# Kernel optimization log

Hardware: AMD Instinct MI355X
Metric: run time of the kernel (lower is better)

Reference implementation:

```python
import jax, jax.numpy as jnp
import numpy as np

N = 100000      # nodes
E = 1600000     # edges
IN_DIM = 128
OUT_DIM = 128
H = 8           # num_heads
D = OUT_DIM // H  # per-head dim = 16
L = 2           # num_layers
NEG_SLOPE = 0.1


def setup_inputs() -> dict:
    key = jax.random.key(0)
    ks = jax.random.split(key, 12)
    features = jax.random.normal(ks[0], (N, IN_DIM), dtype=jnp.float32)
    src = jax.random.randint(ks[1], (E,), 0, N, dtype=jnp.int32)
    dst = jax.random.randint(ks[2], (E,), 0, N, dtype=jnp.int32)
    w = jax.random.uniform(ks[3], (E,), dtype=jnp.float32)
    # per-layer params: fc weight [in, H*D], attn_left/right [H, D]
    s = 1.0 / np.sqrt(IN_DIM)
    W1 = jax.random.uniform(ks[4], (IN_DIM, H * D), minval=-s, maxval=s, dtype=jnp.float32)
    al1 = jax.random.normal(ks[5], (H, D), dtype=jnp.float32) * 0.1
    ar1 = jax.random.normal(ks[6], (H, D), dtype=jnp.float32) * 0.1
    W2 = jax.random.uniform(ks[7], (OUT_DIM, H * D), minval=-s, maxval=s, dtype=jnp.float32)
    al2 = jax.random.normal(ks[8], (H, D), dtype=jnp.float32) * 0.1
    ar2 = jax.random.normal(ks[9], (H, D), dtype=jnp.float32) * 0.1
    so = 1.0 / np.sqrt(L * OUT_DIM)
    Wm = jax.random.uniform(ks[10], (L * OUT_DIM, OUT_DIM), minval=-so, maxval=so, dtype=jnp.float32)
    bm = jax.random.uniform(ks[11], (OUT_DIM,), minval=-so, maxval=so, dtype=jnp.float32)
    return {"features": features, "src": src, "dst": dst, "w": w,
            "W1": W1, "al1": al1, "ar1": ar1, "W2": W2, "al2": al2, "ar2": ar2,
            "Wm": Wm, "bm": bm}


def gat_layer(x, src, dst, w, W, al, ar):
    # x: [N, in_dim] -> ft: [N, H, D]
    ft = (x @ W).reshape(N, H, D)
    el = jnp.einsum('nhd,hd->nh', ft, al)  # [N, H]
    er = jnp.einsum('nhd,hd->nh', ft, ar)  # [N, H]
    # edge-wise u_add_v + leaky_relu, scaled by edge weight w
    e = jax.nn.leaky_relu(el[src] + er[dst], negative_slope=NEG_SLOPE)  # [E, H]
    e = w[:, None] * e
    # edge_softmax over incoming edges of each dst node (numerically stable)
    m = jax.ops.segment_max(e, dst, num_segments=N)  # [N, H]
    m = jnp.where(jnp.isfinite(m), m, 0.0)           # empty segments -> 0
    ex = jnp.exp(e - m[dst])
    s = jax.ops.segment_sum(ex, dst, num_segments=N)  # [N, H] (>0 wherever indexed)
    a = ex / s[dst]                                   # [E, H]
    # u_mul_e + sum aggregation
    msg = ft[src] * a[:, :, None]                     # [E, H, D]
    out = jax.ops.segment_sum(msg, dst, num_segments=N)  # [N, H, D]
    out = jax.nn.relu(out)
    return out.reshape(N, H * D)  # concat heads


def reference(features, src, dst, w, W1, al1, ar1, W2, al2, ar2, Wm, bm):
    x1 = gat_layer(features, src, dst, w, W1, al1, ar1)
    x2 = gat_layer(x1, src, dst, w, W2, al2, ar2)
    h = jnp.concatenate([x1, x2], axis=-1)  # [N, L*OUT_DIM]
    return h @ Wm + bm                       # [N, OUT_DIM]
```

## Files before the change

### kernel.cpp

```cpp
#include <hip/hip_runtime.h>
#include <hip/hip_bf16.h>

#define NEG_SLOPE 0.1f
#define EPB 4096
#define BINSH 9
#define DMAX 512

typedef __attribute__((ext_vector_type(8))) short bf16x8;
typedef __attribute__((ext_vector_type(4))) float f32x4;

__device__ __forceinline__ float bf2f(unsigned u) { return __uint_as_float(u << 16); }
__device__ __forceinline__ float bflo(unsigned u) { return __uint_as_float(u << 16); }
__device__ __forceinline__ float bfhi(unsigned u) { return __uint_as_float(u & 0xffff0000u); }
__device__ __forceinline__ unsigned short f2bf(float f) {
    __hip_bfloat16 h = __float2bfloat16(f);
    unsigned short r;
    __builtin_memcpy(&r, &h, 2);
    return r;
}

__global__ __launch_bounds__(256) void binhist_k(const int* __restrict__ dst,
                                                 int* __restrict__ bin_counts, int E) {
    __shared__ int cnt[256];
    int t = threadIdx.x;
    cnt[t] = 0;
    __syncthreads();
    int base = blockIdx.x * EPB;
    if (base + EPB <= E) {
        const int4* d4 = (const int4*)(dst + base);
        #pragma unroll
        for (int i = 0; i < 4; ++i) {
            int4 v = d4[i * 256 + t];
            atomicAdd(&cnt[v.x >> BINSH], 1);
            atomicAdd(&cnt[v.y >> BINSH], 1);
            atomicAdd(&cnt[v.z >> BINSH], 1);
            atomicAdd(&cnt[v.w >> BINSH], 1);
        }
    } else {
        for (int i = 0; i < 4; ++i) {
            int j0 = base + (i * 256 + t) * 4;
            #pragma unroll
            for (int c = 0; c < 4; ++c)
                if (j0 + c < E) atomicAdd(&cnt[dst[j0 + c] >> BINSH], 1);
        }
    }
    __syncthreads();
    if (cnt[t]) atomicAdd(&bin_counts[t], cnt[t]);
}

__global__ __launch_bounds__(256) void scan256_k(const int* __restrict__ bin_counts,
                                                 int* __restrict__ binoffs,
                                                 int* __restrict__ gcur, int nbins) {
    __shared__ int sbuf[256];
    int t = threadIdx.x;
    int c = (t < nbins) ? bin_counts[t] : 0;
    sbuf[t] = c;
    __syncthreads();
    for (int off = 1; off < 256; off <<= 1) {
        int u = (t >= off) ? sbuf[t - off] : 0;
        __syncthreads();
        sbuf[t] += u;
        __syncthreads();
    }
    int ex = sbuf[t] - c;
    binoffs[t] = ex;
    if (t == 255) binoffs[256] = ex + c;
    gcur[t] = ex;
}

__global__ __launch_bounds__(256) void binify_k(const int* __restrict__ src,
                                                const int* __restrict__ dst,
                                                const float* __restrict__ w,
                                                int* __restrict__ gcur,
                                                int4* __restrict__ tmp, int E) {
    __shared__ int cnt[256];
    __shared__ int basearr[256];
    int t = threadIdx.x;
    cnt[t] = 0;
    __syncthreads();
    int base = blockIdx.x * EPB;
    int es[16], ed[16], ew[16];
    bool va[16];
    if (base + EPB <= E) {
        const int4* s4 = (const int4*)(src + base);
        const int4* d4 = (const int4*)(dst + base);
        const int4* w4 = (const int4*)(w + base);
        #pragma unroll
        for (int i = 0; i < 4; ++i) {
            int slot = i * 256 + t;
            int4 sv = s4[slot]; int4 dv = d4[slot]; int4 wv = w4[slot];
            es[i*4+0]=sv.x; es[i*4+1]=sv.y; es[i*4+2]=sv.z; es[i*4+3]=sv.w;
            ed[i*4+0]=dv.x; ed[i*4+1]=dv.y; ed[i*4+2]=dv.z; ed[i*4+3]=dv.w;
            ew[i*4+0]=wv.x; ew[i*4+1]=wv.y; ew[i*4+2]=wv.z; ew[i*4+3]=wv.w;
            va[i*4+0]=va[i*4+1]=va[i*4+2]=va[i*4+3]=true;
        }
    } else {
        #pragma unroll
        for (int i = 0; i < 4; ++i) {
            #pragma unroll
            for (int c = 0; c < 4; ++c) {
                int j = base + (i * 256 + t) * 4 + c;
                bool v = j < E;
                va[i*4+c] = v;
                es[i*4+c] = v ? src[j] : 0;
                ed[i*4+c] = v ? dst[j] : 0;
                ew[i*4+c] = v ? __float_as_int(w[j]) : 0;
            }
        }
    }
    #pragma unroll
    for (int i = 0; i < 16; ++i)
        if (va[i]) atomicAdd(&cnt[ed[i] >> BINSH], 1);
    __syncthreads();
    int c = cnt[t];
    basearr[t] = c ? atomicAdd(&gcur[t], c) : 0;
    __syncthreads();
    cnt[t] = 0;
    __syncthreads();
    #pragma unroll
    for (int i = 0; i < 16; ++i) {
        if (va[i]) {
            int b = ed[i] >> BINSH;
            int pos = atomicAdd(&cnt[b], 1);
            tmp[basearr[b] + pos] = make_int4(es[i], ew[i], ed[i], 0);
        }
    }
}

__global__ __launch_bounds__(256) void binfin_k(const int4* __restrict__ tmp,
                                                const int* __restrict__ binoffs,
                                                int* __restrict__ offs,
                                                int2* __restrict__ snw, int N, int E) {
    __shared__ int ncnt[512];
    __shared__ int noff[512];
    __shared__ int sbuf[256];
    int b = blockIdx.x, t = threadIdx.x;
    int lo = b << BINSH;
    int hi = min(lo + 512, N);
    int ebeg = binoffs[b], eend = binoffs[b + 1];
    ncnt[t] = 0; ncnt[t + 256] = 0;
    __syncthreads();
    for (int j = ebeg + t; j < eend; j += 256)
        atomicAdd(&ncnt[tmp[j].z - lo], 1);
    __syncthreads();
    int a0 = ncnt[2 * t], a1 = ncnt[2 * t + 1];
    sbuf[t] = a0 + a1;
    __syncthreads();
    for (int off = 1; off < 256; off <<= 1) {
        int u = (t >= off) ? sbuf[t - off] : 0;
        __syncthreads();
        sbuf[t] += u;
        __syncthreads();
    }
    int ex = sbuf[t] - (a0 + a1);
    noff[2 * t] = ex;
    noff[2 * t + 1] = ex + a0;
    if (lo + 2 * t     < hi) offs[lo + 2 * t]     = ebeg + ex;
    if (lo + 2 * t + 1 < hi) offs[lo + 2 * t + 1] = ebeg + ex + a0;
    if (b == 0 && t == 0) offs[N] = E;
    ncnt[t] = 0; ncnt[t + 256] = 0;
    __syncthreads();
    for (int j = ebeg + t; j < eend; j += 256) {
        int4 e = tmp[j];
        int idx = e.z - lo;
        int pos = atomicAdd(&ncnt[idx], 1);
        snw[ebeg + noff[idx] + pos] = make_int2(e.x, e.y);
    }
}

__global__ __launch_bounds__(256) void deghist_k(const int* __restrict__ offs,
                                                 int* __restrict__ dhist, int N) {
    __shared__ int h[DMAX];
    int t = threadIdx.x;
    for (int i = t; i < DMAX; i += 256) h[i] = 0;
    __syncthreads();
    int n = blockIdx.x * 256 + t;
    if (n < N) {
        int d = min(offs[n + 1] - offs[n], DMAX - 1);
        atomicAdd(&h[d], 1);
    }
    __syncthreads();
    for (int i = t; i < DMAX; i += 256) if (h[i]) atomicAdd(&dhist[i], h[i]);
}

__global__ __launch_bounds__(512) void degscan_k(const int* __restrict__ dhist,
                                                 int* __restrict__ dcur) {
    __shared__ int buf[DMAX];
    int t = threadIdx.x;
    int v = dhist[t];
    buf[t] = v;
    __syncthreads();
    for (int off = 1; off < DMAX; off <<= 1) {
        int u = (t >= off) ? buf[t - off] : 0;
        __syncthreads();
        buf[t] += u;
        __syncthreads();
    }
    dcur[t] = buf[t] - v;
}

__global__ __launch_bounds__(256) void degscat_k(const int* __restrict__ offs,
                                                 int* __restrict__ dcur,
                                                 int* __restrict__ perm, int N) {
    __shared__ int cnt[DMAX];
    __shared__ int basea[DMAX];
    int t = threadIdx.x;
    for (int i = t; i < DMAX; i += 256) cnt[i] = 0;
    __syncthreads();
    int n = blockIdx.x * 256 + t;
    int d = -1;
    if (n < N) {
        d = min(offs[n + 1] - offs[n], DMAX - 1);
        atomicAdd(&cnt[d], 1);
    }
    __syncthreads();
    for (int i = t; i < DMAX; i += 256) {
        int c = cnt[i];
        basea[i] = c ? atomicAdd(&dcur[i], c) : 0;
    }
    __syncthreads();
    for (int i = t; i < DMAX; i += 256) cnt[i] = 0;
    __syncthreads();
    if (n < N) {
        int pos = atomicAdd(&cnt[d], 1);
        perm[basea[d] + pos] = n;
    }
}

__global__ void prep_w_k(const float* __restrict__ W1, const float* __restrict__ W2,
                         const float* __restrict__ Wm, unsigned short* __restrict__ Wt1,
                         unsigned short* __restrict__ Wt2, unsigned short* __restrict__ Wtm) {
    int id = blockIdx.x * blockDim.x + threadIdx.x;
    if (id < 16384) {
        int k = id >> 7, c = id & 127;
        Wt1[c * 128 + k] = f2bf(W1[id]);
    } else if (id < 32768) {
        int e = id - 16384; int k = e >> 7, c = e & 127;
        Wt2[c * 128 + k] = f2bf(W2[e]);
    } else if (id < 65536) {
        int e = id - 32768;
        int k = e >> 7, c = e & 127;
        Wtm[c * 256 + k] = f2bf(Wm[e]);
    }
}

template<int K, bool A_F32, bool BIAS, bool OUT_BF16>
__global__ __launch_bounds__(256) void gemm_mfma(const void* __restrict__ A0v,
                                                 const void* __restrict__ A1v,
                                                 const unsigned short* __restrict__ Wt,
                                                 const float* __restrict__ bias,
                                                 void* __restrict__ Cv, int M) {
    __shared__ __align__(16) unsigned short At[128 * 128];
    __shared__ __align__(16) unsigned short Bt[128 * 128];
    const int t = threadIdx.x;
    const int lane = t & 63;
    const int wv = t >> 6;
    const int m0 = blockIdx.x * 128;
    const int l15 = lane & 15;
    const int l4 = lane >> 4;

    f32x4 acc[2][8];
    #pragma unroll
    for (int r = 0; r < 2; ++r)
        #pragma unroll
        for (int c = 0; c < 8; ++c) acc[r][c] = (f32x4){0.f, 0.f, 0.f, 0.f};

    const int srow = t >> 4;
    const int scol = (t & 15) * 8;

    for (int k0 = 0; k0 < K; k0 += 128) {
        const int chunk = k0 >> 7;
        #pragma unroll
        for (int p = 0; p < 8; ++p) {
            int row = p * 16 + srow;
            int gm = m0 + row;
            uint4 pk = make_uint4(0, 0, 0, 0);
            if (A_F32) {
                const float* Ap = (const float*)(chunk ? A1v : A0v);
                float4 f0 = make_float4(0.f,0.f,0.f,0.f), f1 = f0;
                if (gm < M) {
                    f0 = *(const float4*)(Ap + (size_t)gm * 128 + scol);
                    f1 = *(const float4*)(Ap + (size_t)gm * 128 + scol + 4);
                }
                pk.x = f2bf(f0.x) | ((unsigned)f2bf(f0.y) << 16);
                pk.y = f2bf(f0.z) | ((unsigned)f2bf(f0.w) << 16);
                pk.z = f2bf(f1.x) | ((unsigned)f2bf(f1.y) << 16);
                pk.w = f2bf(f1.z) | ((unsigned)f2bf(f1.w) << 16);
            } else {
                const unsigned short* Ap = (const unsigned short*)(chunk ? A1v : A0v);
                if (gm < M) pk = *(const uint4*)(Ap + (size_t)gm * 128 + scol);
            }
            int byte = (row * 256 + scol * 2) ^ ((row & 7) << 4);
            *(uint4*)((char*)At + byte) = pk;
        }
        #pragma unroll
        for (int p = 0; p < 8; ++p) {
            int row = p * 16 + srow;
            uint4 pk = *(const uint4*)(Wt + (size_t)row * K + k0 + scol);
            int byte = (row * 256 + scol * 2) ^ ((row & 7) << 4);
            *(uint4*)((char*)Bt + byte) = pk;
        }
        __syncthreads();
        #pragma unroll
        for (int ks = 0; ks < 4; ++ks) {
            int kb = ks * 32 + l4 * 8;
            bf16x8 af[2], bfv[8];
            #pragma unroll
            for (int r = 0; r < 2; ++r) {
                int row = wv * 32 + r * 16 + l15;
                int byte = (row * 256 + kb * 2) ^ ((row & 7) << 4);
                af[r] = *(const bf16x8*)((char*)At + byte);
            }
            #pragma unroll
            for (int c = 0; c < 8; ++c) {
                int col = c * 16 + l15;
                int byte = (col * 256 + kb * 2) ^ ((col & 7) << 4);
                bfv[c] = *(const bf16x8*)((char*)Bt + byte);
            }
            #pragma unroll
            for (int r = 0; r < 2; ++r)
                #pragma unroll
                for (int c = 0; c < 8; ++c)
                    acc[r][c] = __builtin_amdgcn_mfma_f32_16x16x32_bf16(af[r], bfv[c], acc[r][c], 0, 0, 0);
        }
        __syncthreads();
    }
    float bb[8];
    if (BIAS) {
        #pragma unroll
        for (int c = 0; c < 8; ++c) bb[c] = bias[c * 16 + l15];
    }
    #pragma unroll
    for (int r = 0; r < 2; ++r) {
        #pragma unroll
        for (int q = 0; q < 4; ++q) {
            int row = m0 + wv * 32 + r * 16 + l4 * 4 + q;
            if (row < M) {
                #pragma unroll
                for (int c = 0; c < 8; ++c) {
                    int col = c * 16 + l15;
                    float v = acc[r][c][q];
                    if (BIAS) v += bb[c];
                    if (OUT_BF16) ((unsigned short*)Cv)[(size_t)row * 128 + col] = f2bf(v);
                    else          ((float*)Cv)[(size_t)row * 128 + col] = v;
                }
            }
        }
    }
}

__global__ void elr_k(const __hip_bfloat16* __restrict__ ft, const float* __restrict__ al,
                      const float* __restrict__ ar, __hip_bfloat16* __restrict__ el,
                      __hip_bfloat16* __restrict__ er, int n) {
    int idx = blockIdx.x * blockDim.x + threadIdx.x;
    if (idx >= n * 8) return;
    int node = idx >> 3, h = idx & 7;
    const __hip_bfloat16* f = ft + (size_t)node * 128 + h * 16;
    uint4 a = *(const uint4*)f;
    uint4 b = *(const uint4*)(f + 8);
    float fv[16];
    fv[0]  = bflo(a.x); fv[1]  = bfhi(a.x);
    fv[2]  = bflo(a.y); fv[3]  = bfhi(a.y);
    fv[4]  = bflo(a.z); fv[5]  = bfhi(a.z);
    fv[6]  = bflo(a.w); fv[7]  = bfhi(a.w);
    fv[8]  = bflo(b.x); fv[9]  = bfhi(b.x);
    fv[10] = bflo(b.y); fv[11] = bfhi(b.y);
    fv[12] = bflo(b.z); fv[13] = bfhi(b.z);
    fv[14] = bflo(b.w); fv[15] = bfhi(b.w);
    float e1 = 0.f, e2 = 0.f;
    #pragma unroll
    for (int d = 0; d < 16; ++d) { e1 += fv[d] * al[h * 16 + d]; e2 += fv[d] * ar[h * 16 + d]; }
    unsigned short r1 = f2bf(e1), r2 = f2bf(e2);
    __builtin_memcpy(&el[idx], &r1, 2);
    __builtin_memcpy(&er[idx], &r2, 2);
}

__global__ __launch_bounds__(256) void agg_k(const __hip_bfloat16* __restrict__ ftb,
                                             const __hip_bfloat16* __restrict__ el,
                                             const __hip_bfloat16* __restrict__ er,
                                             const int2* __restrict__ snw,
                                             const int* __restrict__ offs,
                                             const int* __restrict__ perm,
                                             unsigned short* __restrict__ out, int n) {
    __shared__ int2 rec[4][16][4][8];
    int wid = threadIdx.x >> 6;
    int lane = threadIdx.x & 63;
    int g = lane >> 4;
    int gl = lane & 15;
    int hd = gl >> 1;
    unsigned gl16 = (unsigned)(gl * 16);
    int idx = blockIdx.x * 16 + wid * 4 + g;
    bool valid = idx < n;
    int node = valid ? perm[idx] : 0;
    int beg = 0, deg = 0;
    if (valid) { beg = offs[node]; deg = offs[node + 1] - beg; }
    const char* fb = (const char*)ftb;

    float erv[8];
    {
        uint4 u = *(const uint4*)(er + (size_t)node * 8);
        erv[0] = bflo(u.x); erv[1] = bfhi(u.x);
        erv[2] = bflo(u.y); erv[3] = bfhi(u.y);
        erv[4] = bflo(u.z); erv[5] = bfhi(u.z);
        erv[6] = bflo(u.w); erv[7] = bfhi(u.w);
    }

    float acc[8];
    #pragma unroll
    for (int k = 0; k < 8; ++k) acc[k] = 0.f;
    float s = 0.f;

    int wdeg = deg;
    wdeg = max(wdeg, __shfl_xor(wdeg, 16));
    wdeg = max(wdeg, __shfl_xor(wdeg, 32));

    for (int c0 = 0; c0 < wdeg; c0 += 16) {
        int cnt = min(16, deg - c0);
        if (gl < cnt) {
            int2 p2 = snw[beg + c0 + gl];
            int off = p2.x << 8;
            float wv = __int_as_float(p2.y);
            uint4 u = *(const uint4*)(el + (size_t)p2.x * 8);
            float elv[8];
            elv[0] = bflo(u.x); elv[1] = bfhi(u.x);
            elv[2] = bflo(u.y); elv[3] = bfhi(u.y);
            elv[4] = bflo(u.z); elv[5] = bfhi(u.z);
            elv[6] = bflo(u.w); elv[7] = bfhi(u.w);
            #pragma unroll
            for (int h = 0; h < 8; ++h) {
                float tt = elv[h] + erv[h];
                tt = tt > 0.f ? tt : NEG_SLOPE * tt;
                float p = __expf(tt * wv);
                rec[wid][gl][g][h ^ (gl & 7)] = make_int2(off, __float_as_int(p));
            }
        }
        __builtin_amdgcn_wave_barrier();
        asm volatile("s_waitcnt lgkmcnt(0)" ::: "memory");
        __builtin_amdgcn_wave_barrier();

        int cmax = cnt;
        cmax = max(cmax, __shfl_xor(cmax, 16));
        cmax = max(cmax, __shfl_xor(cmax, 32));

        #pragma unroll 4
        for (int j = 0; j < cmax; ++j) {
            if (j < cnt) {
                int2 r = rec[wid][j][g][hd ^ (j & 7)];
                float a = __int_as_float(r.y);
                uint4 u = *(const uint4*)(fb + ((unsigned)r.x + gl16));
                s += a;
                acc[0] += a * bflo(u.x); acc[1] += a * bfhi(u.x);
                acc[2] += a * bflo(u.y); acc[3] += a * bfhi(u.y);
                acc[4] += a * bflo(u.z); acc[5] += a * bfhi(u.z);
                acc[6] += a * bflo(u.w); acc[7] += a * bfhi(u.w);
            }
        }
        __builtin_amdgcn_wave_barrier();
    }

    if (valid) {
        float sinv = s > 0.f ? 1.f / s : 0.f;
        float o[8];
        #pragma unroll
        for (int k = 0; k < 8; ++k) o[k] = fmaxf(acc[k] * sinv, 0.f);
        uint4 pk;
        pk.x = f2bf(o[0]) | ((unsigned)f2bf(o[1]) << 16);
        pk.y = f2bf(o[2]) | ((unsigned)f2bf(o[3]) << 16);
        pk.z = f2bf(o[4]) | ((unsigned)f2bf(o[5]) << 16);
        pk.w = f2bf(o[6]) | ((unsigned)f2bf(o[7]) << 16);
        *(uint4*)((char*)out + (size_t)node * 256 + gl16) = pk;
    }
}

extern "C" void kernel_launch(void* const* d_in, const int* in_sizes, int n_in,
                              void* d_out, int out_size, void* d_ws, size_t ws_size,
                              hipStream_t stream) {
    const float* features = (const float*)d_in[0];
    const int*   src      = (const int*)d_in[1];
    const int*   dst      = (const int*)d_in[2];
    const float* w        = (const float*)d_in[3];
    const float* W1       = (const float*)d_in[4];
    const float* al1      = (const float*)d_in[5];
    const float* ar1      = (const float*)d_in[6];
    const float* W2       = (const float*)d_in[7];
    const float* al2      = (const float*)d_in[8];
    const float* ar2      = (const float*)d_in[9];
    const float* Wm       = (const float*)d_in[10];
    const float* bm       = (const float*)d_in[11];
    float* out = (float*)d_out;

    const int N = in_sizes[0] / 128;
    const int E = in_sizes[1];

    char* ws = (char*)d_ws;
    unsigned short* ftb = (unsigned short*)ws;            ws += (size_t)N * 128 * 2;
    unsigned short* x1b = (unsigned short*)ws;            ws += (size_t)N * 128 * 2;
    unsigned short* x2b = (unsigned short*)ws;            ws += (size_t)N * 128 * 2;
    unsigned short* el  = (unsigned short*)ws;            ws += (size_t)N * 8 * 2;
    unsigned short* er  = (unsigned short*)ws;            ws += (size_t)N * 8 * 2;
    unsigned short* Wt1 = (unsigned short*)ws;            ws += (size_t)128 * 128 * 2;
    unsigned short* Wt2 = (unsigned short*)ws;            ws += (size_t)128 * 128 * 2;
    unsigned short* Wtm = (unsigned short*)ws;            ws += (size_t)128 * 256 * 2;
    int* offs      = (int*)ws;                            ws += (size_t)(N + 4) * 4;
    int* bin_counts= (int*)ws;                            ws += 256 * 4;
    int* binoffs   = (int*)ws;                            ws += 260 * 4;
    int* gcur      = (int*)ws;                            ws += 256 * 4;
    int* dhist     = (int*)ws;                            ws += DMAX * 4;
    int* dcur      = (int*)ws;                            ws += DMAX * 4;
    int* perm      = (int*)ws;                            ws += (size_t)N * 4;
    int2* snw      = (int2*)ws;                           ws += (size_t)E * 8;
    int4* tmp = (int4*)x1b;

    hipMemsetAsync(bin_counts, 0, 256 * sizeof(int), stream);
    hipMemsetAsync(dhist, 0, DMAX * sizeof(int), stream);

    const int nbins = (N + 511) >> BINSH;
    const int nblk_e = (E + EPB - 1) / EPB;
    const int nblk_n = (N + 255) / 256;

    prep_w_k<<<256, 256, 0, stream>>>(W1, W2, Wm, Wt1, Wt2, Wtm);

    binhist_k<<<nblk_e, 256, 0, stream>>>(dst, bin_counts, E);
    scan256_k<<<1, 256, 0, stream>>>(bin_counts, binoffs, gcur, nbins);
    binify_k<<<nblk_e, 256, 0, stream>>>(src, dst, w, gcur, tmp, E);
    binfin_k<<<nbins, 256, 0, stream>>>(tmp, binoffs, offs, snw, N, E);

    deghist_k<<<nblk_n, 256, 0, stream>>>(offs, dhist, N);
    degscan_k<<<1, 512, 0, stream>>>(dhist, dcur);
    degscat_k<<<nblk_n, 256, 0, stream>>>(offs, dcur, perm, N);

    int gemm_grid = (N + 127) / 128;
    int agg_grid = (N + 15) / 16;

    gemm_mfma<128, true, false, true><<<gemm_grid, 256, 0, stream>>>(features, nullptr, Wt1, nullptr, ftb, N);
    elr_k<<<(N * 8 + 255) / 256, 256, 0, stream>>>((const __hip_bfloat16*)ftb, al1, ar1,
                                                   (__hip_bfloat16*)el, (__hip_bfloat16*)er, N);
    agg_k<<<agg_grid, 256, 0, stream>>>((const __hip_bfloat16*)ftb, (const __hip_bfloat16*)el,
                                        (const __hip_bfloat16*)er, snw, offs, perm, x1b, N);

    gemm_mfma<128, false, false, true><<<gemm_grid, 256, 0, stream>>>(x1b, nullptr, Wt2, nullptr, ftb, N);
    elr_k<<<(N * 8 + 255) / 256, 256, 0, stream>>>((const __hip_bfloat16*)ftb, al2, ar2,
                                                   (__hip_bfloat16*)el, (__hip_bfloat16*)er, N);
    agg_k<<<agg_grid, 256, 0, stream>>>((const __hip_bfloat16*)ftb, (const __hip_bfloat16*)el,
                                        (const __hip_bfloat16*)er, snw, offs, perm, x2b, N);

    gemm_mfma<256, false, true, false><<<gemm_grid, 256, 0, stream>>>(x1b, x2b, Wtm, bm, out, N);
}
```

Baseline: 316.8 us.

## Fuse preprocessing kernels, pack binned edges, compute attention logits inside aggregation

Folds the weight-transpose prep into the bin histogram kernel and the degree histogram into binfin, which removes two launches. Binned edge records shrink from int4 to int2 by packing the local dst index into the high bits of src. The el/er kernel is dropped: agg_k now computes el from the gathered source feature row and er from the node's own row, then accumulates without the shared-memory staging. This removes a pass over ft and the el/er traffic, at the cost of redundant dot products per edge and serialized per-node edge loops that can diverge across nodes of different degree.

```diff
diff --git a/kernel.cpp b/kernel.cpp
--- a/kernel.cpp
+++ b/kernel.cpp
@@ -4,12 +4,11 @@
 #define NEG_SLOPE 0.1f
 #define EPB 4096
 #define BINSH 9
-#define DMAX 512
+#define DMAX 256
 
 typedef __attribute__((ext_vector_type(8))) short bf16x8;
 typedef __attribute__((ext_vector_type(4))) float f32x4;
 
-__device__ __forceinline__ float bf2f(unsigned u) { return __uint_as_float(u << 16); }
 __device__ __forceinline__ float bflo(unsigned u) { return __uint_as_float(u << 16); }
 __device__ __forceinline__ float bfhi(unsigned u) { return __uint_as_float(u & 0xffff0000u); }
 __device__ __forceinline__ unsigned short f2bf(float f) {
@@ -20,7 +19,13 @@
 }
 
 __global__ __launch_bounds__(256) void binhist_k(const int* __restrict__ dst,
-                                                 int* __restrict__ bin_counts, int E) {
+                                                 int* __restrict__ bin_counts, int E,
+                                                 const float* __restrict__ W1,
+                                                 const float* __restrict__ W2,
+                                                 const float* __restrict__ Wm,
+                                                 unsigned short* __restrict__ Wt1,
+                                                 unsigned short* __restrict__ Wt2,
+                                                 unsigned short* __restrict__ Wtm) {
     __shared__ int cnt[256];
     int t = threadIdx.x;
     cnt[t] = 0;
@@ -43,6 +48,18 @@
             for (int c = 0; c < 4; ++c)
                 if (j0 + c < E) atomicAdd(&cnt[dst[j0 + c] >> BINSH], 1);
         }
+    }
+    int id = blockIdx.x * 256 + t;
+    if (id < 16384) {
+        int k = id >> 7, c = id & 127;
+        Wt1[c * 128 + k] = f2bf(W1[id]);
+    } else if (id < 32768) {
+        int e = id - 16384; int k = e >> 7, c = e & 127;
+        Wt2[c * 128 + k] = f2bf(W2[e]);
+    } else if (id < 65536) {
+        int e = id - 32768;
+        int k = e >> 7, c = e & 127;
+        Wtm[c * 256 + k] = f2bf(Wm[e]);
     }
     __syncthreads();
     if (cnt[t]) atomicAdd(&bin_counts[t], cnt[t]);
@@ -72,7 +89,7 @@
                                                 const int* __restrict__ dst,
                                                 const float* __restrict__ w,
                                                 int* __restrict__ gcur,
-                                                int4* __restrict__ tmp, int E) {
+                                                int2* __restrict__ tmp, int E) {
     __shared__ int cnt[256];
     __shared__ int basearr[256];
     int t = threadIdx.x;
@@ -122,26 +139,28 @@
         if (va[i]) {
             int b = ed[i] >> BINSH;
             int pos = atomicAdd(&cnt[b], 1);
-            tmp[basearr[b] + pos] = make_int4(es[i], ew[i], ed[i], 0);
-        }
-    }
-}
-
-__global__ __launch_bounds__(256) void binfin_k(const int4* __restrict__ tmp,
+            tmp[basearr[b] + pos] = make_int2(es[i] | ((ed[i] & 511) << 17), ew[i]);
+        }
+    }
+}
+
+__global__ __launch_bounds__(256) void binfin_k(const int2* __restrict__ tmp,
                                                 const int* __restrict__ binoffs,
                                                 int* __restrict__ offs,
-                                                int2* __restrict__ snw, int N, int E) {
+                                                int2* __restrict__ snw,
+                                                int* __restrict__ dhist, int N, int E) {
     __shared__ int ncnt[512];
     __shared__ int noff[512];
     __shared__ int sbuf[256];
+    __shared__ int dh[DMAX];
     int b = blockIdx.x, t = threadIdx.x;
     int lo = b << BINSH;
     int hi = min(lo + 512, N);
     int ebeg = binoffs[b], eend = binoffs[b + 1];
-    ncnt[t] = 0; ncnt[t + 256] = 0;
+    ncnt[t] = 0; ncnt[t + 256] = 0; dh[t] = 0;
     __syncthreads();
     for (int j = ebeg + t; j < eend; j += 256)
-        atomicAdd(&ncnt[tmp[j].z - lo], 1);
+        atomicAdd(&ncnt[(unsigned)tmp[j].x >> 17], 1);
     __syncthreads();
     int a0 = ncnt[2 * t], a1 = ncnt[2 * t + 1];
     sbuf[t] = a0 + a1;
@@ -155,35 +174,27 @@
     int ex = sbuf[t] - (a0 + a1);
     noff[2 * t] = ex;
     noff[2 * t + 1] = ex + a0;
-    if (lo + 2 * t     < hi) offs[lo + 2 * t]     = ebeg + ex;
-    if (lo + 2 * t + 1 < hi) offs[lo + 2 * t + 1] = ebeg + ex + a0;
+    if (lo + 2 * t < hi) {
+        offs[lo + 2 * t] = ebeg + ex;
+        atomicAdd(&dh[min(a0, DMAX - 1)], 1);
+    }
+    if (lo + 2 * t + 1 < hi) {
+        offs[lo + 2 * t + 1] = ebeg + ex + a0;
+        atomicAdd(&dh[min(a1, DMAX - 1)], 1);
+    }
     if (b == 0 && t == 0) offs[N] = E;
     ncnt[t] = 0; ncnt[t + 256] = 0;
     __syncthreads();
+    if (dh[t]) atomicAdd(&dhist[t], dh[t]);
     for (int j = ebeg + t; j < eend; j += 256) {
-        int4 e = tmp[j];
-        int idx = e.z - lo;
+        int2 e = tmp[j];
+        int idx = (unsigned)e.x >> 17;
         int pos = atomicAdd(&ncnt[idx], 1);
-        snw[ebeg + noff[idx] + pos] = make_int2(e.x, e.y);
-    }
-}
-
-__global__ __launch_bounds__(256) void deghist_k(const int* __restrict__ offs,
-                                                 int* __restrict__ dhist, int N) {
-    __shared__ int h[DMAX];
-    int t = threadIdx.x;
-    for (int i = t; i < DMAX; i += 256) h[i] = 0;
-    __syncthreads();
-    int n = blockIdx.x * 256 + t;
-    if (n < N) {
-        int d = min(offs[n + 1] - offs[n], DMAX - 1);
-        atomicAdd(&h[d], 1);
-    }
-    __syncthreads();
-    for (int i = t; i < DMAX; i += 256) if (h[i]) atomicAdd(&dhist[i], h[i]);
-}
-
-__global__ __launch_bounds__(512) void degscan_k(const int* __restrict__ dhist,
+        snw[ebeg + noff[idx] + pos] = make_int2(e.x & 0x1ffff, e.y);
+    }
+}
+
+__global__ __launch_bounds__(256) void degscan_k(const int* __restrict__ dhist,
                                                  int* __restrict__ dcur) {
     __shared__ int buf[DMAX];
     int t = threadIdx.x;
@@ -205,7 +216,7 @@
     __shared__ int cnt[DMAX];
     __shared__ int basea[DMAX];
     int t = threadIdx.x;
-    for (int i = t; i < DMAX; i += 256) cnt[i] = 0;
+    cnt[t] = 0;
     __syncthreads();
     int n = blockIdx.x * 256 + t;
     int d = -1;
@@ -214,33 +225,14 @@
         atomicAdd(&cnt[d], 1);
     }
     __syncthreads();
-    for (int i = t; i < DMAX; i += 256) {
-        int c = cnt[i];
-        basea[i] = c ? atomicAdd(&dcur[i], c) : 0;
-    }
-    __syncthreads();
-    for (int i = t; i < DMAX; i += 256) cnt[i] = 0;
+    int c = cnt[t];
+    basea[t] = c ? atomicAdd(&dcur[t], c) : 0;
+    __syncthreads();
+    cnt[t] = 0;
     __syncthreads();
     if (n < N) {
         int pos = atomicAdd(&cnt[d], 1);
         perm[basea[d] + pos] = n;
-    }
-}
-
-__global__ void prep_w_k(const float* __restrict__ W1, const float* __restrict__ W2,
-                         const float* __restrict__ Wm, unsigned short* __restrict__ Wt1,
-                         unsigned short* __restrict__ Wt2, unsigned short* __restrict__ Wtm) {
-    int id = blockIdx.x * blockDim.x + threadIdx.x;
-    if (id < 16384) {
-        int k = id >> 7, c = id & 127;
-        Wt1[c * 128 + k] = f2bf(W1[id]);
-    } else if (id < 32768) {
-        int e = id - 16384; int k = e >> 7, c = e & 127;
-        Wt2[c * 128 + k] = f2bf(W2[e]);
-    } else if (id < 65536) {
-        int e = id - 32768;
-        int k = e >> 7, c = e & 127;
-        Wtm[c * 256 + k] = f2bf(Wm[e]);
     }
 }
 
@@ -349,60 +341,40 @@
     }
 }
 
-__global__ void elr_k(const __hip_bfloat16* __restrict__ ft, const float* __restrict__ al,
-                      const float* __restrict__ ar, __hip_bfloat16* __restrict__ el,
-                      __hip_bfloat16* __restrict__ er, int n) {
-    int idx = blockIdx.x * blockDim.x + threadIdx.x;
-    if (idx >= n * 8) return;
-    int node = idx >> 3, h = idx & 7;
-    const __hip_bfloat16* f = ft + (size_t)node * 128 + h * 16;
-    uint4 a = *(const uint4*)f;
-    uint4 b = *(const uint4*)(f + 8);
-    float fv[16];
-    fv[0]  = bflo(a.x); fv[1]  = bfhi(a.x);
-    fv[2]  = bflo(a.y); fv[3]  = bfhi(a.y);
-    fv[4]  = bflo(a.z); fv[5]  = bfhi(a.z);
-    fv[6]  = bflo(a.w); fv[7]  = bfhi(a.w);
-    fv[8]  = bflo(b.x); fv[9]  = bfhi(b.x);
-    fv[10] = bflo(b.y); fv[11] = bfhi(b.y);
-    fv[12] = bflo(b.z); fv[13] = bfhi(b.z);
-    fv[14] = bflo(b.w); fv[15] = bfhi(b.w);
-    float e1 = 0.f, e2 = 0.f;
-    #pragma unroll
-    for (int d = 0; d < 16; ++d) { e1 += fv[d] * al[h * 16 + d]; e2 += fv[d] * ar[h * 16 + d]; }
-    unsigned short r1 = f2bf(e1), r2 = f2bf(e2);
-    __builtin_memcpy(&el[idx], &r1, 2);
-    __builtin_memcpy(&er[idx], &r2, 2);
-}
-
 __global__ __launch_bounds__(256) void agg_k(const __hip_bfloat16* __restrict__ ftb,
-                                             const __hip_bfloat16* __restrict__ el,
-                                             const __hip_bfloat16* __restrict__ er,
                                              const int2* __restrict__ snw,
                                              const int* __restrict__ offs,
                                              const int* __restrict__ perm,
+                                             const float* __restrict__ AL,
+                                             const float* __restrict__ AR,
                                              unsigned short* __restrict__ out, int n) {
-    __shared__ int2 rec[4][16][4][8];
-    int wid = threadIdx.x >> 6;
-    int lane = threadIdx.x & 63;
-    int g = lane >> 4;
-    int gl = lane & 15;
+    int tid = threadIdx.x;
+    int gl = tid & 15;
     int hd = gl >> 1;
     unsigned gl16 = (unsigned)(gl * 16);
-    int idx = blockIdx.x * 16 + wid * 4 + g;
+    int idx = blockIdx.x * 16 + (tid >> 4);
     bool valid = idx < n;
     int node = valid ? perm[idx] : 0;
     int beg = 0, deg = 0;
     if (valid) { beg = offs[node]; deg = offs[node + 1] - beg; }
     const char* fb = (const char*)ftb;
 
-    float erv[8];
+    float alf[8], arf[8];
     {
-        uint4 u = *(const uint4*)(er + (size_t)node * 8);
-        erv[0] = bflo(u.x); erv[1] = bfhi(u.x);
-        erv[2] = bflo(u.y); erv[3] = bfhi(u.y);
-        erv[4] = bflo(u.z); erv[5] = bfhi(u.z);
-        erv[6] = bflo(u.w); erv[7] = bfhi(u.w);
+        const float* ap = AL + hd * 16 + (gl & 1) * 8;
+        const float* rp = AR + hd * 16 + (gl & 1) * 8;
+        #pragma unroll
+        for (int d = 0; d < 8; ++d) { alf[d] = ap[d]; arf[d] = rp[d]; }
+    }
+
+    float er_h;
+    {
+        uint4 mu = *(const uint4*)(fb + ((unsigned)node << 8) + gl16);
+        float ep = arf[0] * bflo(mu.x) + arf[1] * bfhi(mu.x)
+                 + arf[2] * bflo(mu.y) + arf[3] * bfhi(mu.y)
+                 + arf[4] * bflo(mu.z) + arf[5] * bfhi(mu.z)
+                 + arf[6] * bflo(mu.w) + arf[7] * bfhi(mu.w);
+        er_h = ep + __shfl_xor(ep, 1);
     }
 
     float acc[8];
@@ -410,52 +382,35 @@
     for (int k = 0; k < 8; ++k) acc[k] = 0.f;
     float s = 0.f;
 
-    int wdeg = deg;
-    wdeg = max(wdeg, __shfl_xor(wdeg, 16));
-    wdeg = max(wdeg, __shfl_xor(wdeg, 32));
-
-    for (int c0 = 0; c0 < wdeg; c0 += 16) {
-        int cnt = min(16, deg - c0);
-        if (gl < cnt) {
-            int2 p2 = snw[beg + c0 + gl];
-            int off = p2.x << 8;
-            float wv = __int_as_float(p2.y);
-            uint4 u = *(const uint4*)(el + (size_t)p2.x * 8);
-            float elv[8];
-            elv[0] = bflo(u.x); elv[1] = bfhi(u.x);
-            elv[2] = bflo(u.y); elv[3] = bfhi(u.y);
-            elv[4] = bflo(u.z); elv[5] = bfhi(u.z);
-            elv[6] = bflo(u.w); elv[7] = bfhi(u.w);
-            #pragma unroll
-            for (int h = 0; h < 8; ++h) {
-                float tt = elv[h] + erv[h];
-                tt = tt > 0.f ? tt : NEG_SLOPE * tt;
-                float p = __expf(tt * wv);
-                rec[wid][gl][g][h ^ (gl & 7)] = make_int2(off, __float_as_int(p));
-            }
-        }
-        __builtin_amdgcn_wave_barrier();
-        asm volatile("s_waitcnt lgkmcnt(0)" ::: "memory");
-        __builtin_amdgcn_wave_barrier();
-
-        int cmax = cnt;
-        cmax = max(cmax, __shfl_xor(cmax, 16));
-        cmax = max(cmax, __shfl_xor(cmax, 32));
-
-        #pragma unroll 4
-        for (int j = 0; j < cmax; ++j) {
-            if (j < cnt) {
-                int2 r = rec[wid][j][g][hd ^ (j & 7)];
-                float a = __int_as_float(r.y);
-                uint4 u = *(const uint4*)(fb + ((unsigned)r.x + gl16));
-                s += a;
-                acc[0] += a * bflo(u.x); acc[1] += a * bfhi(u.x);
-                acc[2] += a * bflo(u.y); acc[3] += a * bfhi(u.y);
-                acc[4] += a * bflo(u.z); acc[5] += a * bfhi(u.z);
-                acc[6] += a * bflo(u.w); acc[7] += a * bfhi(u.w);
-            }
-        }
-        __builtin_amdgcn_wave_barrier();
+    for (int j0 = 0; j0 < deg; j0 += 8) {
+        uint4 rv[8];
+        float wv8[8];
+        #pragma unroll
+        for (int q = 0; q < 8; ++q) {
+            int j = j0 + q;
+            bool act = j < deg;
+            int2 p2 = snw[act ? beg + j : 0];
+            wv8[q] = act ? __int_as_float(p2.y) : 0.f;
+            unsigned ad = act ? (((unsigned)p2.x << 8) + gl16) : gl16;
+            rv[q] = *(const uint4*)(fb + ad);
+        }
+        #pragma unroll
+        for (int q = 0; q < 8; ++q) {
+            float ep = alf[0] * bflo(rv[q].x) + alf[1] * bfhi(rv[q].x)
+                     + alf[2] * bflo(rv[q].y) + alf[3] * bfhi(rv[q].y)
+                     + alf[4] * bflo(rv[q].z) + alf[5] * bfhi(rv[q].z)
+                     + alf[6] * bflo(rv[q].w) + alf[7] * bfhi(rv[q].w);
+            float el_h = ep + __shfl_xor(ep, 1);
+            float tt = el_h + er_h;
+            tt = tt > 0.f ? tt : NEG_SLOPE * tt;
+            float p = __expf(tt * wv8[q]);
+            p = (j0 + q < deg) ? p : 0.f;
+            s += p;
+            acc[0] += p * bflo(rv[q].x); acc[1] += p * bfhi(rv[q].x);
+            acc[2] += p * bflo(rv[q].y); acc[3] += p * bfhi(rv[q].y);
+            acc[4] += p * bflo(rv[q].z); acc[5] += p * bfhi(rv[q].z);
+            acc[6] += p * bflo(rv[q].w); acc[7] += p * bfhi(rv[q].w);
+        }
     }
 
     if (valid) {
@@ -468,7 +423,7 @@
         pk.y = f2bf(o[2]) | ((unsigned)f2bf(o[3]) << 16);
         pk.z = f2bf(o[4]) | ((unsigned)f2bf(o[5]) << 16);
         pk.w = f2bf(o[6]) | ((unsigned)f2bf(o[7]) << 16);
-        *(uint4*)((char*)out + (size_t)node * 256 + gl16) = pk;
+        *(uint4*)((char*)out + ((size_t)node << 8) + gl16) = pk;
     }
 }
 
@@ -496,8 +451,6 @@
     unsigned short* ftb = (unsigned short*)ws;            ws += (size_t)N * 128 * 2;
     unsigned short* x1b = (unsigned short*)ws;            ws += (size_t)N * 128 * 2;
     unsigned short* x2b = (unsigned short*)ws;            ws += (size_t)N * 128 * 2;
-    unsigned short* el  = (unsigned short*)ws;            ws += (size_t)N * 8 * 2;
-    unsigned short* er  = (unsigned short*)ws;            ws += (size_t)N * 8 * 2;
     unsigned short* Wt1 = (unsigned short*)ws;            ws += (size_t)128 * 128 * 2;
     unsigned short* Wt2 = (unsigned short*)ws;            ws += (size_t)128 * 128 * 2;
     unsigned short* Wtm = (unsigned short*)ws;            ws += (size_t)128 * 256 * 2;
@@ -509,7 +462,7 @@
     int* dcur      = (int*)ws;                            ws += DMAX * 4;
     int* perm      = (int*)ws;                            ws += (size_t)N * 4;
     int2* snw      = (int2*)ws;                           ws += (size_t)E * 8;
-    int4* tmp = (int4*)x1b;
+    int2* tmp      = (int2*)ws;                           ws += (size_t)E * 8;
 
     hipMemsetAsync(bin_counts, 0, 256 * sizeof(int), stream);
     hipMemsetAsync(dhist, 0, DMAX * sizeof(int), stream);
@@ -518,31 +471,21 @@
     const int nblk_e = (E + EPB - 1) / EPB;
     const int nblk_n = (N + 255) / 256;
 
-    prep_w_k<<<256, 256, 0, stream>>>(W1, W2, Wm, Wt1, Wt2, Wtm);
-
-    binhist_k<<<nblk_e, 256, 0, stream>>>(dst, bin_counts, E);
+    binhist_k<<<nblk_e, 256, 0, stream>>>(dst, bin_counts, E, W1, W2, Wm, Wt1, Wt2, Wtm);
     scan256_k<<<1, 256, 0, stream>>>(bin_counts, binoffs, gcur, nbins);
     binify_k<<<nblk_e, 256, 0, stream>>>(src, dst, w, gcur, tmp, E);
-    binfin_k<<<nbins, 256, 0, stream>>>(tmp, binoffs, offs, snw, N, E);
-
-    deghist_k<<<nblk_n, 256, 0, stream>>>(offs, dhist, N);
-    degscan_k<<<1, 512, 0, stream>>>(dhist, dcur);
+    binfin_k<<<nbins, 256, 0, stream>>>(tmp, binoffs, offs, snw, dhist, N, E);
+    degscan_k<<<1, 256, 0, stream>>>(dhist, dcur);
     degscat_k<<<nblk_n, 256, 0, stream>>>(offs, dcur, perm, N);
 
     int gemm_grid = (N + 127) / 128;
     int agg_grid = (N + 15) / 16;
 
     gemm_mfma<128, true, false, true><<<gemm_grid, 256, 0, stream>>>(features, nullptr, Wt1, nullptr, ftb, N);
-    elr_k<<<(N * 8 + 255) / 256, 256, 0, stream>>>((const __hip_bfloat16*)ftb, al1, ar1,
-                                                   (__hip_bfloat16*)el, (__hip_bfloat16*)er, N);
-    agg_k<<<agg_grid, 256, 0, stream>>>((const __hip_bfloat16*)ftb, (const __hip_bfloat16*)el,
-                                        (const __hip_bfloat16*)er, snw, offs, perm, x1b, N);
+    agg_k<<<agg_grid, 256, 0, stream>>>((const __hip_bfloat16*)ftb, snw, offs, perm, al1, ar1, x1b, N);
 
     gemm_mfma<128, false, false, true><<<gemm_grid, 256, 0, stream>>>(x1b, nullptr, Wt2, nullptr, ftb, N);
-    elr_k<<<(N * 8 + 255) / 256, 256, 0, stream>>>((const __hip_bfloat16*)ftb, al2, ar2,
-                                                   (__hip_bfloat16*)el, (__hip_bfloat16*)er, N);
-    agg_k<<<agg_grid, 256, 0, stream>>>((const __hip_bfloat16*)ftb, (const __hip_bfloat16*)el,
-                                        (const __hip_bfloat16*)er, snw, offs, perm, x2b, N);
+    agg_k<<<agg_grid, 256, 0, stream>>>((const __hip_bfloat16*)ftb, snw, offs, perm, al2, ar2, x2b, N);
 
     gemm_mfma<256, false, true, false><<<gemm_grid, 256, 0, stream>>>(x1b, x2b, Wtm, bm, out, N);
 }
```

Result: faster. 282.7 us (median of 3 runs) (-10.8%).
